# Optimization experiments

Measured on AMD Instinct MI355X. Metric: run time of the kernel, lower is better.

The kernel has to match this reference:

```python
import jax, jax.numpy as jnp
import numpy as np


def _conv1x1(x, w, b):
    # x: [B, Cin, T, H, W], w: [Cout, Cin], b: [Cout] -> [B, Cout, T, H, W]
    return jnp.einsum('bcthw,oc->bothw', x, w) + b[None, :, None, None, None]


def setup_inputs() -> dict:
    key = jax.random.key(0)
    ks = jax.random.split(key, 9)
    B, Ci, T, H, W = 2, 128, 4, 32, 32
    Co = 64
    s_in = 1.0 / np.sqrt(Ci)
    s_out = 1.0 / np.sqrt(Co)
    return {
        'z': jax.random.normal(ks[0], (B, Ci, T, H, W), dtype=jnp.float32),
        'w_theta': jax.random.uniform(ks[1], (Co, Ci), jnp.float32, -s_in, s_in),
        'b_theta': jax.random.uniform(ks[2], (Co,), jnp.float32, -s_in, s_in),
        'w_phi': jax.random.uniform(ks[3], (Co, Ci), jnp.float32, -s_in, s_in),
        'b_phi': jax.random.uniform(ks[4], (Co,), jnp.float32, -s_in, s_in),
        'w_psi': jax.random.uniform(ks[5], (Co, Ci), jnp.float32, -s_in, s_in),
        'b_psi': jax.random.uniform(ks[6], (Co,), jnp.float32, -s_in, s_in),
        'w_v': jax.random.uniform(ks[7], (Ci, Co), jnp.float32, -s_out, s_out),
        'b_v': jax.random.uniform(ks[8], (Ci,), jnp.float32, -s_out, s_out),
    }


def reference(z, w_theta, b_theta, w_phi, b_phi, w_psi, b_psi, w_v, b_v):
    B, Ci, T, H, W = z.shape
    Co = w_theta.shape[0]
    N = T * H * W
    # 1x1 conv projections, flattened to [B, Co, N]
    theta = _conv1x1(z, w_theta, b_theta).reshape(B, Co, N)
    phi = _conv1x1(z, w_phi, b_phi).reshape(B, Co, N)
    psi = _conv1x1(z, w_psi, b_psi).reshape(B, Co, N)
    # g = phi^T @ psi : [B, N, N]; normalize with ReLU(g / N)
    g = jnp.einsum('bcn,bcm->bnm', phi, psi)
    norm_g = jax.nn.relu(g / jnp.asarray(N, z.dtype))
    # tmp = norm_g @ theta^T -> [B, N, Co] -> [B, Co, T, H, W]
    tmp = jnp.einsum('bnm,bcm->bcn', norm_g, theta).reshape(B, Co, T, H, W)
    vg = _conv1x1(tmp, w_v, b_v)
    return vg + z
```

## Files before the change

kernel.cpp:

```cpp
#include <hip/hip_runtime.h>


#define NSEQ 4096
#define CI 128
#define CO 64

typedef __attribute__((ext_vector_type(8))) short bf16x8;
typedef __attribute__((ext_vector_type(4))) short bf16x4;
typedef __attribute__((ext_vector_type(4))) float f32x4;

static __device__ inline short f2bf(float f) {
  union { float f; unsigned u; } v; v.f = f;
  unsigned r = v.u + 0x7fffu + ((v.u >> 16) & 1u);
  return (short)(r >> 16);
}

#define MFMA32(a, b, c) __builtin_amdgcn_mfma_f32_16x16x32_bf16(a, b, c, 0, 0, 0)

#if __has_builtin(__builtin_amdgcn_mfma_f32_16x16x16bf16_1k)
static __device__ inline f32x4 mfma16(bf16x4 a, bf16x4 b, f32x4 c) {
  return __builtin_amdgcn_mfma_f32_16x16x16bf16_1k(a, b, c, 0, 0, 0);
}
#else
static __device__ inline f32x4 mfma16(bf16x4 a, bf16x4 b, f32x4 c) {
  asm("v_mfma_f32_16x16x16_bf16 %0, %1, %2, %0" : "+v"(c) : "v"(a), "v"(b));
  return c;
}
#endif

__global__ __launch_bounds__(256, 2) void proj_kernel(
    const float* __restrict__ z,
    const float* __restrict__ w_th, const float* __restrict__ b_th,
    const float* __restrict__ w_ph, const float* __restrict__ b_ph,
    const float* __restrict__ w_ps, const float* __restrict__ b_ps,
    short* __restrict__ Qg, short* __restrict__ Kg, short* __restrict__ Vt)
{
  const int bid = blockIdx.x;
  const int b = bid >> 8;
  const int n0 = (bid & 255) * 16;
  const int t = threadIdx.x;
  const int w = t >> 6, l = t & 63, lr = l & 15, lg = l >> 4;
  const f32x4 zero4 = {0.f, 0.f, 0.f, 0.f};

  bf16x8 zf[4];
#pragma unroll
  for (int ks = 0; ks < 4; ++ks) {
    const float* zp = z + (size_t)(b * CI + ks * 32 + lg * 8) * NSEQ + n0 + lr;
    float tmp[8];
#pragma unroll
    for (int j = 0; j < 8; ++j) tmp[j] = zp[(size_t)j * NSEQ];
#pragma unroll
    for (int j = 0; j < 8; ++j) zf[ks][j] = f2bf(tmp[j]);
  }

  {
    const float* Wm[2] = {w_ph, w_ps};
    const float* Bm[2] = {b_ph, b_ps};
    short*       Dm[2] = {Qg, Kg};
#pragma unroll
    for (int mt = 0; mt < 2; ++mt) {
      f32x4 acc = zero4;
#pragma unroll
      for (int ks = 0; ks < 4; ++ks) {
        const float* wp = Wm[mt] + (size_t)(w * 16 + lr) * CI + ks * 32 + lg * 8;
        f32x4 x0 = *(const f32x4*)wp;
        f32x4 x1 = *(const f32x4*)(wp + 4);
        bf16x8 wf;
#pragma unroll
        for (int j = 0; j < 4; ++j) { wf[j] = f2bf(x0[j]); wf[4 + j] = f2bf(x1[j]); }
        acc = MFMA32(wf, zf[ks], acc);
      }
      const f32x4 bias4 = *(const f32x4*)(Bm[mt] + w * 16 + lg * 4);
      bf16x4 pk;
#pragma unroll
      for (int r = 0; r < 4; ++r) pk[r] = f2bf(acc[r] + bias4[r]);
      *(bf16x4*)(Dm[mt] + (size_t)(b * NSEQ + n0 + lr) * CO + w * 16 + lg * 4) = pk;
    }
  }

  {
    f32x4 acc = zero4;
#pragma unroll
    for (int ks = 0; ks < 4; ++ks) {
      const float* wp = w_th + (size_t)(w * 16 + lr) * CI + ks * 32 + lg * 8;
      f32x4 x0 = *(const f32x4*)wp;
      f32x4 x1 = *(const f32x4*)(wp + 4);
      bf16x8 wtf;
#pragma unroll
      for (int j = 0; j < 4; ++j) { wtf[j] = f2bf(x0[j]); wtf[4 + j] = f2bf(x1[j]); }
      acc = MFMA32(zf[ks], wtf, acc);
    }
    const float bias = b_th[w * 16 + lr];
    bf16x4 pk;
#pragma unroll
    for (int r = 0; r < 4; ++r) pk[r] = f2bf(acc[r] + bias);
    *(bf16x4*)(Vt + (size_t)(b * CO + w * 16 + lr) * NSEQ + n0 + lg * 4) = pk;
  }
}

__global__ __launch_bounds__(256, 4) void attn_kernel(
    const short* __restrict__ Qg, const short* __restrict__ Kg,
    const short* __restrict__ Vt, float* __restrict__ Opart)
{
  __shared__ f32x4 smem4[32768 / 16];
  char* smem = (char*)smem4;
  char* Km = smem;
  char* Vm = smem + 16384;

  const int bid = blockIdx.x;
  const int grp = bid & 7;
  const int nt = bid >> 3;
  const int b = grp >> 2, msi = grp & 3;
  const int n0 = nt * 32;
  const int m_base = msi * 1024;
  const int t = threadIdx.x;
  const int w = t >> 6, l = t & 63, lr = l & 15, lg = l >> 4;
  const f32x4 zero4 = {0.f, 0.f, 0.f, 0.f};

  bf16x8 q[2][2];
#pragma unroll
  for (int nsub = 0; nsub < 2; ++nsub) {
    const short* qp = Qg + (size_t)(b * NSEQ + n0 + nsub * 16 + lr) * CO + lg * 8;
    q[nsub][0] = *(const bf16x8*)qp;
    q[nsub][1] = *(const bf16x8*)(qp + 32);
  }

  f32x4 oacc[4][2];
#pragma unroll
  for (int i = 0; i < 4; ++i)
#pragma unroll
    for (int j = 0; j < 2; ++j) oacc[i][j] = zero4;

  bf16x8 stg[8];
  auto load_stage = [&](int ss) {
    const int m0 = m_base + ss * 128;
#pragma unroll
    for (int r = 0; r < 4; ++r) {
      const int ck = r * 256 + t;
      stg[r] = *(const bf16x8*)(Kg + (size_t)(b * NSEQ + m0 + (ck >> 3)) * CO + (ck & 7) * 8);
    }
#pragma unroll
    for (int r = 0; r < 4; ++r) {
      const int cv = r * 256 + t;
      stg[4 + r] = *(const bf16x8*)(Vt + (size_t)(b * CO + (cv >> 4)) * NSEQ + m0 + (cv & 15) * 8);
    }
  };
  auto write_stage = [&]() {
#pragma unroll
    for (int r = 0; r < 4; ++r) {
      const int ck = r * 256 + t, m = ck >> 3, c8 = ck & 7;
      *(bf16x8*)(Km + m * 128 + ((c8 ^ (m & 7)) * 16)) = stg[r];
    }
#pragma unroll
    for (int r = 0; r < 4; ++r) {
      const int cv = r * 256 + t, o = cv >> 4, mc = cv & 15;
      *(bf16x8*)(Vm + o * 256 + ((mc ^ (o & 7)) * 16)) = stg[4 + r];
    }
  };

  load_stage(0);
  write_stage();
  __syncthreads();

  for (int ss = 0; ss < 8; ++ss) {
    if (ss < 7) load_stage(ss + 1);

#pragma unroll
    for (int msub = 0; msub < 2; ++msub) {
      const int mr = w * 32 + msub * 16 + lr;
      bf16x8 k0 = *(const bf16x8*)(Km + mr * 128 + ((lg ^ (mr & 7)) * 16));
      bf16x8 k1 = *(const bf16x8*)(Km + mr * 128 + (((4 + lg) ^ (mr & 7)) * 16));
      bf16x4 pf[2];
#pragma unroll
      for (int nsub = 0; nsub < 2; ++nsub) {
        f32x4 s = MFMA32(k0, q[nsub][0], zero4);
        s = MFMA32(k1, q[nsub][1], s);
#pragma unroll
        for (int r = 0; r < 4; ++r) {
          const float p = s[r] > 0.f ? s[r] * (1.f / 4096.f) : 0.f;
          pf[nsub][r] = f2bf(p);
        }
      }
      const int vchunk = w * 4 + msub * 2 + (lg >> 1);
      const int voff = (lg & 1) * 8;
#pragma unroll
      for (int osub = 0; osub < 4; ++osub) {
        const int orow = osub * 16 + lr;
        bf16x4 vf = *(const bf16x4*)(Vm + orow * 256 + ((vchunk ^ (orow & 7)) * 16) + voff);
        oacc[osub][0] = mfma16(vf, pf[0], oacc[osub][0]);
        oacc[osub][1] = mfma16(vf, pf[1], oacc[osub][1]);
      }
    }

    __syncthreads();
    if (ss < 7) {
      write_stage();
      __syncthreads();
    }
  }

  float* part = (float*)smem;
  {
    float* dst = part + w * 2048;
#pragma unroll
    for (int osub = 0; osub < 4; ++osub)
#pragma unroll
      for (int nsub = 0; nsub < 2; ++nsub)
#pragma unroll
        for (int r = 0; r < 4; ++r)
          dst[(osub * 16 + lg * 4 + r) * 32 + nsub * 16 + lr] = oacc[osub][nsub][r];
  }
  __syncthreads();
  {
    float* gout = Opart + (((size_t)(b * 128 + nt) * 4 + msi) * 2048);
#pragma unroll
    for (int pass = 0; pass < 2; ++pass) {
      const int o = w * 16 + pass * 8 + (l >> 3);
      const int nq = (l & 7) * 4;
      f32x4 s = *(const f32x4*)(part + o * 32 + nq);
#pragma unroll
      for (int p = 1; p < 4; ++p)
        s += *(const f32x4*)(part + p * 2048 + o * 32 + nq);
      *(f32x4*)(gout + o * 32 + nq) = s;
    }
  }
}

__global__ __launch_bounds__(256, 2) void epi_kernel(
    const float* __restrict__ Opart, const float* __restrict__ w_v,
    const float* __restrict__ b_v, const float* __restrict__ z,
    float* __restrict__ out)
{
  __shared__ float Olds[64 * 16];

  const int bid = blockIdx.x;
  const int b = bid >> 8;
  const int n16 = bid & 255;
  const int n0 = n16 * 16;
  const int t = threadIdx.x;

  {
    const float* src = Opart + ((size_t)(b * 128 + (n16 >> 1)) * 4) * 2048 + (n16 & 1) * 16;
    const int o = t >> 2, nq = (t & 3) * 4;
    f32x4 s = *(const f32x4*)(src + o * 32 + nq);
#pragma unroll
    for (int p = 1; p < 4; ++p)
      s += *(const f32x4*)(src + (size_t)p * 2048 + o * 32 + nq);
    *(f32x4*)(Olds + o * 16 + nq) = s;
  }
  __syncthreads();

  const int w = t >> 6, l = t & 63, lr = l & 15, lg = l >> 4;
  const f32x4 zero4 = {0.f, 0.f, 0.f, 0.f};

  bf16x4 of[4];
#pragma unroll
  for (int osub = 0; osub < 4; ++osub)
#pragma unroll
    for (int j = 0; j < 4; ++j)
      of[osub][j] = f2bf(Olds[(osub * 16 + lg * 4 + j) * 16 + lr]);

#pragma unroll
  for (int c2 = 0; c2 < 2; ++c2) {
    const int cis = w * 2 + c2;
    f32x4 e = zero4;
#pragma unroll
    for (int osub = 0; osub < 4; ++osub) {
      f32x4 wl = *(const f32x4*)(w_v + (size_t)(cis * 16 + lr) * CO + osub * 16 + lg * 4);
      bf16x4 wf;
#pragma unroll
      for (int j = 0; j < 4; ++j) wf[j] = f2bf(wl[j]);
      e = mfma16(wf, of[osub], e);
    }
    const f32x4 bv = *(const f32x4*)(b_v + cis * 16 + lg * 4);
#pragma unroll
    for (int r = 0; r < 4; ++r) {
      const int ci = cis * 16 + lg * 4 + r;
      const size_t off = (size_t)(b * CI + ci) * NSEQ + n0 + lr;
      out[off] = e[r] + z[off] + bv[r];
    }
  }
}

extern "C" void kernel_launch(void* const* d_in, const int* in_sizes, int n_in,
                              void* d_out, int out_size, void* d_ws, size_t ws_size,
                              hipStream_t stream) {
  const float* z    = (const float*)d_in[0];
  const float* w_th = (const float*)d_in[1];
  const float* b_th = (const float*)d_in[2];
  const float* w_ph = (const float*)d_in[3];
  const float* b_ph = (const float*)d_in[4];
  const float* w_ps = (const float*)d_in[5];
  const float* b_ps = (const float*)d_in[6];
  const float* w_v  = (const float*)d_in[7];
  const float* b_v  = (const float*)d_in[8];
  float* out = (float*)d_out;

  short* Qg = (short*)d_ws;
  short* Kg = Qg + 2 * NSEQ * CO;
  short* Vt = Kg + 2 * NSEQ * CO;
  float* Opart = (float*)((char*)d_ws + 3u * 1024 * 1024);

  proj_kernel<<<512, 256, 0, stream>>>(z, w_th, b_th, w_ph, b_ph, w_ps, b_ps,
                                       Qg, Kg, Vt);
  attn_kernel<<<1024, 256, 0, stream>>>(Qg, Kg, Vt, Opart);
  epi_kernel<<<512, 256, 0, stream>>>(Opart, w_v, b_v, z, out);
}
```

Before: 105.8 us.

## Rewrite attention kernel with 32x32 MFMA, register-resident K/V and bf16 partials

The attention kernel is rewritten to use 32x32x16 bf16 MFMA tiles, with each block covering 64 query rows and splitting the key range 8 ways. K and V are loaded straight from global memory into registers, so the LDS staging and per-stage barriers are gone. The P fragments are repacked with v_cvt_pk_bf16 and v_permlane32_swap. The 1/N scale is folded into the phi weights in the projection, and the partial outputs are stored as bf16, which halves partial traffic but costs some precision. The epilogue now sums 8 bf16 partials and processes 32 columns per block.

```diff
diff --git a/kernel.cpp b/kernel.cpp
--- a/kernel.cpp
+++ b/kernel.cpp
@@ -8,14 +8,20 @@
 typedef __attribute__((ext_vector_type(8))) short bf16x8;
 typedef __attribute__((ext_vector_type(4))) short bf16x4;
 typedef __attribute__((ext_vector_type(4))) float f32x4;
+typedef __attribute__((ext_vector_type(16))) float f32x16;
 
 static __device__ inline short f2bf(float f) {
   union { float f; unsigned u; } v; v.f = f;
   unsigned r = v.u + 0x7fffu + ((v.u >> 16) & 1u);
   return (short)(r >> 16);
 }
-
-#define MFMA32(a, b, c) __builtin_amdgcn_mfma_f32_16x16x32_bf16(a, b, c, 0, 0, 0)
+static __device__ inline float bf2f(short s) {
+  union { unsigned u; float f; } v; v.u = ((unsigned)(unsigned short)s) << 16;
+  return v.f;
+}
+
+#define MFMA1632(a, b, c) __builtin_amdgcn_mfma_f32_16x16x32_bf16(a, b, c, 0, 0, 0)
+#define MFMA3216(a, b, c) __builtin_amdgcn_mfma_f32_32x32x16_bf16(a, b, c, 0, 0, 0)
 
 #if __has_builtin(__builtin_amdgcn_mfma_f32_16x16x16bf16_1k)
 static __device__ inline f32x4 mfma16(bf16x4 a, bf16x4 b, f32x4 c) {
@@ -27,6 +33,15 @@
   return c;
 }
 #endif
+
+static __device__ inline unsigned cvt_pk_bf16(float lo, float hi) {
+  unsigned d;
+  asm("v_cvt_pk_bf16_f32 %0, %1, %2" : "=v"(d) : "v"(lo), "v"(hi));
+  return d;
+}
+static __device__ inline void pl32swap(unsigned& a, unsigned& b) {
+  asm("v_permlane32_swap_b32 %0, %1" : "+v"(a), "+v"(b));
+}
 
 __global__ __launch_bounds__(256, 2) void proj_kernel(
     const float* __restrict__ z,
@@ -59,6 +74,7 @@
     short*       Dm[2] = {Qg, Kg};
 #pragma unroll
     for (int mt = 0; mt < 2; ++mt) {
+      const float sc = (mt == 0) ? (1.0f / 4096.0f) : 1.0f;
       f32x4 acc = zero4;
 #pragma unroll
       for (int ks = 0; ks < 4; ++ks) {
@@ -67,13 +83,13 @@
         f32x4 x1 = *(const f32x4*)(wp + 4);
         bf16x8 wf;
 #pragma unroll
-        for (int j = 0; j < 4; ++j) { wf[j] = f2bf(x0[j]); wf[4 + j] = f2bf(x1[j]); }
-        acc = MFMA32(wf, zf[ks], acc);
+        for (int j = 0; j < 4; ++j) { wf[j] = f2bf(x0[j] * sc); wf[4 + j] = f2bf(x1[j] * sc); }
+        acc = MFMA1632(wf, zf[ks], acc);
       }
       const f32x4 bias4 = *(const f32x4*)(Bm[mt] + w * 16 + lg * 4);
       bf16x4 pk;
 #pragma unroll
-      for (int r = 0; r < 4; ++r) pk[r] = f2bf(acc[r] + bias4[r]);
+      for (int r = 0; r < 4; ++r) pk[r] = f2bf(acc[r] + bias4[r] * sc);
       *(bf16x4*)(Dm[mt] + (size_t)(b * NSEQ + n0 + lr) * CO + w * 16 + lg * 4) = pk;
     }
   }
@@ -88,7 +104,7 @@
       bf16x8 wtf;
 #pragma unroll
       for (int j = 0; j < 4; ++j) { wtf[j] = f2bf(x0[j]); wtf[4 + j] = f2bf(x1[j]); }
-      acc = MFMA32(zf[ks], wtf, acc);
+      acc = MFMA1632(zf[ks], wtf, acc);
     }
     const float bias = b_th[w * 16 + lr];
     bf16x4 pk;
@@ -98,186 +114,204 @@
   }
 }
 
-__global__ __launch_bounds__(256, 4) void attn_kernel(
+__global__ __launch_bounds__(256, 3) void attn_kernel(
     const short* __restrict__ Qg, const short* __restrict__ Kg,
-    const short* __restrict__ Vt, float* __restrict__ Opart)
+    const short* __restrict__ Vt, short* __restrict__ Opart)
 {
-  __shared__ f32x4 smem4[32768 / 16];
-  char* smem = (char*)smem4;
-  char* Km = smem;
-  char* Vm = smem + 16384;
+  __shared__ float red[2][4096];
 
   const int bid = blockIdx.x;
-  const int grp = bid & 7;
-  const int nt = bid >> 3;
-  const int b = grp >> 2, msi = grp & 3;
-  const int n0 = nt * 32;
-  const int m_base = msi * 1024;
+  const int ms = bid & 7;
+  const int rr = bid >> 3;
+  const int b  = rr & 1;
+  const int nt = rr >> 1;
+  const int n0 = nt * 64;
   const int t = threadIdx.x;
-  const int w = t >> 6, l = t & 63, lr = l & 15, lg = l >> 4;
-  const f32x4 zero4 = {0.f, 0.f, 0.f, 0.f};
-
-  bf16x8 q[2][2];
-#pragma unroll
-  for (int nsub = 0; nsub < 2; ++nsub) {
-    const short* qp = Qg + (size_t)(b * NSEQ + n0 + nsub * 16 + lr) * CO + lg * 8;
-    q[nsub][0] = *(const bf16x8*)qp;
-    q[nsub][1] = *(const bf16x8*)(qp + 32);
-  }
-
-  f32x4 oacc[4][2];
-#pragma unroll
-  for (int i = 0; i < 4; ++i)
-#pragma unroll
-    for (int j = 0; j < 2; ++j) oacc[i][j] = zero4;
-
-  bf16x8 stg[8];
-  auto load_stage = [&](int ss) {
-    const int m0 = m_base + ss * 128;
-#pragma unroll
-    for (int r = 0; r < 4; ++r) {
-      const int ck = r * 256 + t;
-      stg[r] = *(const bf16x8*)(Kg + (size_t)(b * NSEQ + m0 + (ck >> 3)) * CO + (ck & 7) * 8);
-    }
-#pragma unroll
-    for (int r = 0; r < 4; ++r) {
-      const int cv = r * 256 + t;
-      stg[4 + r] = *(const bf16x8*)(Vt + (size_t)(b * CO + (cv >> 4)) * NSEQ + m0 + (cv & 15) * 8);
-    }
-  };
-  auto write_stage = [&]() {
-#pragma unroll
-    for (int r = 0; r < 4; ++r) {
-      const int ck = r * 256 + t, m = ck >> 3, c8 = ck & 7;
-      *(bf16x8*)(Km + m * 128 + ((c8 ^ (m & 7)) * 16)) = stg[r];
-    }
-#pragma unroll
-    for (int r = 0; r < 4; ++r) {
-      const int cv = r * 256 + t, o = cv >> 4, mc = cv & 15;
-      *(bf16x8*)(Vm + o * 256 + ((mc ^ (o & 7)) * 16)) = stg[4 + r];
-    }
-  };
-
-  load_stage(0);
-  write_stage();
+  const int w = t >> 6, l = t & 63, lc = l & 31, h = l >> 5;
+  const int mw = ms * 512 + w * 128;
+
+  bf16x8 qf[2][4];
+  {
+    const short* qb = Qg + (size_t)(b * NSEQ + n0 + lc) * CO + h * 8;
+#pragma unroll
+    for (int nsub = 0; nsub < 2; ++nsub)
+#pragma unroll
+      for (int ks = 0; ks < 4; ++ks)
+        qf[nsub][ks] = *(const bf16x8*)(qb + (size_t)nsub * 32 * CO + ks * 16);
+  }
+
+  f32x16 oacc[2][2];
+#pragma unroll
+  for (int i = 0; i < 2; ++i)
+#pragma unroll
+    for (int j = 0; j < 2; ++j)
+#pragma unroll
+      for (int e = 0; e < 16; ++e) oacc[i][j][e] = 0.f;
+
+#pragma unroll
+  for (int it = 0; it < 4; ++it) {
+    const int m0 = mw + it * 32;
+
+    bf16x8 kf[4];
+    {
+      const short* kb = Kg + (size_t)(b * NSEQ + m0 + lc) * CO + h * 8;
+#pragma unroll
+      for (int ks = 0; ks < 4; ++ks) kf[ks] = *(const bf16x8*)(kb + ks * 16);
+    }
+
+    f32x16 s0, s1;
+#pragma unroll
+    for (int e = 0; e < 16; ++e) { s0[e] = 0.f; s1[e] = 0.f; }
+#pragma unroll
+    for (int ks = 0; ks < 4; ++ks) s0 = MFMA3216(kf[ks], qf[0][ks], s0);
+    unsigned pk0[8];
+#pragma unroll
+    for (int q = 0; q < 8; ++q)
+      pk0[q] = cvt_pk_bf16(fmaxf(s0[2 * q], 0.f), fmaxf(s0[2 * q + 1], 0.f));
+#pragma unroll
+    for (int ks = 0; ks < 4; ++ks) s1 = MFMA3216(kf[ks], qf[1][ks], s1);
+    unsigned pk1[8];
+#pragma unroll
+    for (int q = 0; q < 8; ++q)
+      pk1[q] = cvt_pk_bf16(fmaxf(s1[2 * q], 0.f), fmaxf(s1[2 * q + 1], 0.f));
+
+    const short* vb = Vt + (size_t)(b * CO + lc) * NSEQ + m0 + h * 8;
+#pragma unroll
+    for (int kw = 0; kw < 2; ++kw) {
+      unsigned x0 = pk0[4 * kw + 0], y0 = pk0[4 * kw + 2];
+      unsigned x1 = pk0[4 * kw + 1], y1 = pk0[4 * kw + 3];
+      pl32swap(x0, y0); pl32swap(x1, y1);
+      union { unsigned u[4]; bf16x8 v; } pb0 = {{x0, x1, y0, y1}};
+      unsigned u0 = pk1[4 * kw + 0], v0 = pk1[4 * kw + 2];
+      unsigned u1 = pk1[4 * kw + 1], v1 = pk1[4 * kw + 3];
+      pl32swap(u0, v0); pl32swap(u1, v1);
+      union { unsigned u[4]; bf16x8 v; } pb1 = {{u0, u1, v0, v1}};
+
+      bf16x8 vf0 = *(const bf16x8*)(vb + kw * 16);
+      bf16x8 vf1 = *(const bf16x8*)(vb + (size_t)32 * NSEQ + kw * 16);
+      oacc[0][0] = MFMA3216(vf0, pb0.v, oacc[0][0]);
+      oacc[1][0] = MFMA3216(vf1, pb0.v, oacc[1][0]);
+      oacc[0][1] = MFMA3216(vf0, pb1.v, oacc[0][1]);
+      oacc[1][1] = MFMA3216(vf1, pb1.v, oacc[1][1]);
+    }
+  }
+
+  if (!(w & 1)) {
+#pragma unroll
+    for (int osub = 0; osub < 2; ++osub)
+#pragma unroll
+      for (int nsub = 0; nsub < 2; ++nsub)
+#pragma unroll
+        for (int rb = 0; rb < 4; ++rb) {
+          f32x4 v;
+#pragma unroll
+          for (int r = 0; r < 4; ++r) v[r] = oacc[osub][nsub][rb * 4 + r];
+          const int o = osub * 32 + rb * 8 + h * 4;
+          const int n = nsub * 32 + lc;
+          const int os = o ^ ((n & 15) << 2);
+          *(f32x4*)&red[w >> 1][n * 64 + os] = v;
+        }
+  }
   __syncthreads();
-
-  for (int ss = 0; ss < 8; ++ss) {
-    if (ss < 7) load_stage(ss + 1);
-
-#pragma unroll
-    for (int msub = 0; msub < 2; ++msub) {
-      const int mr = w * 32 + msub * 16 + lr;
-      bf16x8 k0 = *(const bf16x8*)(Km + mr * 128 + ((lg ^ (mr & 7)) * 16));
-      bf16x8 k1 = *(const bf16x8*)(Km + mr * 128 + (((4 + lg) ^ (mr & 7)) * 16));
-      bf16x4 pf[2];
-#pragma unroll
-      for (int nsub = 0; nsub < 2; ++nsub) {
-        f32x4 s = MFMA32(k0, q[nsub][0], zero4);
-        s = MFMA32(k1, q[nsub][1], s);
-#pragma unroll
-        for (int r = 0; r < 4; ++r) {
-          const float p = s[r] > 0.f ? s[r] * (1.f / 4096.f) : 0.f;
-          pf[nsub][r] = f2bf(p);
+  if (w & 1) {
+#pragma unroll
+    for (int osub = 0; osub < 2; ++osub)
+#pragma unroll
+      for (int nsub = 0; nsub < 2; ++nsub)
+#pragma unroll
+        for (int rb = 0; rb < 4; ++rb) {
+          const int o = osub * 32 + rb * 8 + h * 4;
+          const int n = nsub * 32 + lc;
+          const int os = o ^ ((n & 15) << 2);
+          float* p = &red[w >> 1][n * 64 + os];
+          f32x4 v = *(f32x4*)p;
+#pragma unroll
+          for (int r = 0; r < 4; ++r) v[r] += oacc[osub][nsub][rb * 4 + r];
+          *(f32x4*)p = v;
         }
-      }
-      const int vchunk = w * 4 + msub * 2 + (lg >> 1);
-      const int voff = (lg & 1) * 8;
-#pragma unroll
-      for (int osub = 0; osub < 4; ++osub) {
-        const int orow = osub * 16 + lr;
-        bf16x4 vf = *(const bf16x4*)(Vm + orow * 256 + ((vchunk ^ (orow & 7)) * 16) + voff);
-        oacc[osub][0] = mfma16(vf, pf[0], oacc[osub][0]);
-        oacc[osub][1] = mfma16(vf, pf[1], oacc[osub][1]);
-      }
-    }
-
-    __syncthreads();
-    if (ss < 7) {
-      write_stage();
-      __syncthreads();
-    }
-  }
-
-  float* part = (float*)smem;
-  {
-    float* dst = part + w * 2048;
-#pragma unroll
-    for (int osub = 0; osub < 4; ++osub)
-#pragma unroll
-      for (int nsub = 0; nsub < 2; ++nsub)
-#pragma unroll
-        for (int r = 0; r < 4; ++r)
-          dst[(osub * 16 + lg * 4 + r) * 32 + nsub * 16 + lr] = oacc[osub][nsub][r];
   }
   __syncthreads();
-  {
-    float* gout = Opart + (((size_t)(b * 128 + nt) * 4 + msi) * 2048);
-#pragma unroll
-    for (int pass = 0; pass < 2; ++pass) {
-      const int o = w * 16 + pass * 8 + (l >> 3);
-      const int nq = (l & 7) * 4;
-      f32x4 s = *(const f32x4*)(part + o * 32 + nq);
-#pragma unroll
-      for (int p = 1; p < 4; ++p)
-        s += *(const f32x4*)(part + p * 2048 + o * 32 + nq);
-      *(f32x4*)(gout + o * 32 + nq) = s;
-    }
+
+  short* gout = Opart + (size_t)((b * 64 + nt) * 8 + ms) * 4096;
+#pragma unroll
+  for (int pass = 0; pass < 4; ++pass) {
+    const int lin = pass * 1024 + t * 4;
+    const int n = lin >> 6, os4 = lin & 63;
+    f32x4 v0 = *(f32x4*)&red[0][lin];
+    f32x4 v1 = *(f32x4*)&red[1][lin];
+    const int o = os4 ^ ((n & 15) << 2);
+    bf16x4 pkv;
+#pragma unroll
+    for (int r = 0; r < 4; ++r) pkv[r] = f2bf(v0[r] + v1[r]);
+    *(bf16x4*)(gout + n * 64 + o) = pkv;
   }
 }
 
 __global__ __launch_bounds__(256, 2) void epi_kernel(
-    const float* __restrict__ Opart, const float* __restrict__ w_v,
+    const short* __restrict__ Opart, const float* __restrict__ w_v,
     const float* __restrict__ b_v, const float* __restrict__ z,
     float* __restrict__ out)
 {
-  __shared__ float Olds[64 * 16];
+  __shared__ float Olds[32 * 65];
 
   const int bid = blockIdx.x;
-  const int b = bid >> 8;
-  const int n16 = bid & 255;
-  const int n0 = n16 * 16;
+  const int b = bid >> 7;
+  const int nt32 = bid & 127;
+  const int nt = nt32 >> 1, nh2 = nt32 & 1;
   const int t = threadIdx.x;
 
   {
-    const float* src = Opart + ((size_t)(b * 128 + (n16 >> 1)) * 4) * 2048 + (n16 & 1) * 16;
-    const int o = t >> 2, nq = (t & 3) * 4;
-    f32x4 s = *(const f32x4*)(src + o * 32 + nq);
-#pragma unroll
-    for (int p = 1; p < 4; ++p)
-      s += *(const f32x4*)(src + (size_t)p * 2048 + o * 32 + nq);
-    *(f32x4*)(Olds + o * 16 + nq) = s;
+    const short* src = Opart + (size_t)((b * 64 + nt) * 8) * 4096 + nh2 * 32 * 64;
+    const int n = t >> 3, o8 = (t & 7) * 8;
+    float acc[8];
+#pragma unroll
+    for (int j = 0; j < 8; ++j) acc[j] = 0.f;
+#pragma unroll
+    for (int p = 0; p < 8; ++p) {
+      bf16x8 vv = *(const bf16x8*)(src + (size_t)p * 4096 + n * 64 + o8);
+#pragma unroll
+      for (int j = 0; j < 8; ++j) acc[j] += bf2f(vv[j]);
+    }
+#pragma unroll
+    for (int j = 0; j < 8; ++j) Olds[n * 65 + o8 + j] = acc[j];
   }
   __syncthreads();
 
   const int w = t >> 6, l = t & 63, lr = l & 15, lg = l >> 4;
   const f32x4 zero4 = {0.f, 0.f, 0.f, 0.f};
 
-  bf16x4 of[4];
-#pragma unroll
-  for (int osub = 0; osub < 4; ++osub)
-#pragma unroll
-    for (int j = 0; j < 4; ++j)
-      of[osub][j] = f2bf(Olds[(osub * 16 + lg * 4 + j) * 16 + lr]);
+  bf16x4 of[2][4];
+#pragma unroll
+  for (int nh = 0; nh < 2; ++nh)
+#pragma unroll
+    for (int osub = 0; osub < 4; ++osub)
+#pragma unroll
+      for (int j = 0; j < 4; ++j)
+        of[nh][osub][j] = f2bf(Olds[(nh * 16 + lr) * 65 + osub * 16 + lg * 4 + j]);
 
 #pragma unroll
   for (int c2 = 0; c2 < 2; ++c2) {
     const int cis = w * 2 + c2;
-    f32x4 e = zero4;
+    bf16x4 wfr[4];
 #pragma unroll
     for (int osub = 0; osub < 4; ++osub) {
       f32x4 wl = *(const f32x4*)(w_v + (size_t)(cis * 16 + lr) * CO + osub * 16 + lg * 4);
-      bf16x4 wf;
-#pragma unroll
-      for (int j = 0; j < 4; ++j) wf[j] = f2bf(wl[j]);
-      e = mfma16(wf, of[osub], e);
-    }
-    const f32x4 bv = *(const f32x4*)(b_v + cis * 16 + lg * 4);
-#pragma unroll
-    for (int r = 0; r < 4; ++r) {
-      const int ci = cis * 16 + lg * 4 + r;
-      const size_t off = (size_t)(b * CI + ci) * NSEQ + n0 + lr;
-      out[off] = e[r] + z[off] + bv[r];
+#pragma unroll
+      for (int j = 0; j < 4; ++j) wfr[osub][j] = f2bf(wl[j]);
+    }
+    const f32x4 bv4 = *(const f32x4*)(b_v + cis * 16 + lg * 4);
+#pragma unroll
+    for (int nh = 0; nh < 2; ++nh) {
+      f32x4 e = zero4;
+#pragma unroll
+      for (int osub = 0; osub < 4; ++osub)
+        e = mfma16(wfr[osub], of[nh][osub], e);
+#pragma unroll
+      for (int r = 0; r < 4; ++r) {
+        const int ci = cis * 16 + lg * 4 + r;
+        const size_t off = (size_t)(b * CI + ci) * NSEQ + nt32 * 32 + nh * 16 + lr;
+        out[off] = e[r] + z[off] + bv4[r];
+      }
     }
   }
 }
@@ -299,10 +333,10 @@
   short* Qg = (short*)d_ws;
   short* Kg = Qg + 2 * NSEQ * CO;
   short* Vt = Kg + 2 * NSEQ * CO;
-  float* Opart = (float*)((char*)d_ws + 3u * 1024 * 1024);
+  short* Opart = Vt + 2 * NSEQ * CO;
 
   proj_kernel<<<512, 256, 0, stream>>>(z, w_th, b_th, w_ph, b_ph, w_ps, b_ps,
                                        Qg, Kg, Vt);
   attn_kernel<<<1024, 256, 0, stream>>>(Qg, Kg, Vt, Opart);
-  epi_kernel<<<512, 256, 0, stream>>>(Opart, w_v, b_v, z, out);
-}
+  epi_kernel<<<256, 256, 0, stream>>>(Opart, w_v, b_v, z, out);
+}
```

After: 108.9 us. +3.0%, slower.
